# Performance work log

Measured on AMD Instinct MI355X. Metric: run time of the kernel, lower is better.

## Reference

```python
import jax, jax.numpy as jnp
import numpy as np

N, F_IN, H = 8192, 256, 64


def setup_inputs() -> dict:
    key = jax.random.key(0)
    ks = jax.random.split(key, 5)
    seq1 = jax.random.normal(ks[0], (1, N, F_IN), jnp.float32)
    seq2 = jax.random.normal(ks[1], (1, N, F_IN), jnp.float32)
    # dense (row-stochastic-ish) adjacency, batch dim 1 as in DGI usage
    adj = jax.random.uniform(ks[2], (1, N, N), jnp.float32) / np.float32(N)
    msk = jnp.ones((1, N), jnp.float32)
    # GCN params: Linear(in_ft, out_ft, bias=False) weight [H, F_IN], bias [H], PReLU alpha
    fc_w = jax.random.normal(ks[3], (H, F_IN), jnp.float32) / np.float32(np.sqrt(F_IN))
    gcn_bias = jnp.zeros((H,), jnp.float32)
    prelu_alpha = jnp.array(0.25, jnp.float32)
    # Discriminator: Bilinear(H, H, 1) -> weight [H, H], bias scalar
    disc_w = jax.random.normal(ks[4], (H, H), jnp.float32) / np.float32(np.sqrt(H))
    disc_b = jnp.zeros((1,), jnp.float32)
    return {"seq1": seq1, "seq2": seq2, "adj": adj, "msk": msk,
            "fc_w": fc_w, "gcn_bias": gcn_bias, "prelu_alpha": prelu_alpha,
            "disc_w": disc_w, "disc_b": disc_b}


def _gcn(seq, adj, fc_w, bias, alpha):
    fts = jnp.einsum('bnf,hf->bnh', seq, fc_w)          # linear, no bias
    out = jnp.einsum('bnm,bmh->bnh', adj, fts) + bias   # dense aggregation + bias
    return jnp.where(out > 0, out, alpha * out)          # PReLU


def reference(seq1, seq2, adj, msk, fc_w, gcn_bias, prelu_alpha, disc_w, disc_b):
    h1 = _gcn(seq1, adj, fc_w, gcn_bias, prelu_alpha)    # [1, N, H]
    # AvgReadout with mask: sum(seq*msk,1)/sum(msk)
    c = jnp.sum(h1 * msk[..., None], axis=1) / jnp.sum(msk)  # [1, H]
    c = jax.nn.sigmoid(c)
    h2 = _gcn(seq2, adj, fc_w, gcn_bias, prelu_alpha)    # [1, N, H]
    # Bilinear discriminator: sc[b,n] = h[b,n,:] @ W @ c[b,:] + b
    wc = jnp.einsum('hk,bk->bh', disc_w, c)              # [1, H]
    sc1 = jnp.einsum('bnh,bh->bn', h1, wc) + disc_b[0]   # [1, N]
    sc2 = jnp.einsum('bnh,bh->bn', h2, wc) + disc_b[0]   # [1, N]
    return jnp.concatenate([sc1, sc2], axis=1)           # [1, 2N]
```

## Files before the change

kernel.cpp:

```cpp
#include <hip/hip_runtime.h>
#include <cstdint>
#include <cstddef>

#define NN 8192
#define FIN 256
#define HH 64
#define SPLIT 16
#define KLEN (NN / SPLIT)

typedef float vf4 __attribute__((ext_vector_type(4)));
typedef short vbf8 __attribute__((ext_vector_type(8)));

__device__ inline unsigned pk_trunc(float lo, float hi) {
  return __builtin_amdgcn_perm(__float_as_uint(hi), __float_as_uint(lo), 0x07060302u);
}
__device__ inline unsigned short bf_rne(float x) {
  unsigned u = __float_as_uint(x);
  return (unsigned short)((u + 0x7FFFu + ((u >> 16) & 1u)) >> 16);
}
__device__ inline float bf_to_f(unsigned short s) {
  return __uint_as_float(((unsigned)s) << 16);
}

union FragU { unsigned u[4]; unsigned short s[8]; vbf8 v; };

__device__ inline vbf8 frag_trunc(vf4 a, vf4 b) {
  FragU t;
  t.u[0] = pk_trunc(a[0], a[1]);
  t.u[1] = pk_trunc(a[2], a[3]);
  t.u[2] = pk_trunc(b[0], b[1]);
  t.u[3] = pk_trunc(b[2], b[3]);
  return t.v;
}
__device__ inline vbf8 frag_rne(vf4 a, vf4 b) {
  FragU t;
  t.s[0] = bf_rne(a[0]); t.s[1] = bf_rne(a[1]); t.s[2] = bf_rne(a[2]); t.s[3] = bf_rne(a[3]);
  t.s[4] = bf_rne(b[0]); t.s[5] = bf_rne(b[1]); t.s[6] = bf_rne(b[2]); t.s[7] = bf_rne(b[3]);
  return t.v;
}

__device__ inline void gl_lds16(const void* g, void* l) {
  __builtin_amdgcn_global_load_lds(
      (const __attribute__((address_space(1))) void*)g,
      (__attribute__((address_space(3))) void*)l, 16, 0, 0);
}

__global__ __launch_bounds__(256) void k1_fts(
    const float* __restrict__ seq1, const float* __restrict__ seq2,
    const float* __restrict__ fcw, unsigned short* __restrict__ Bt,
    float* __restrict__ csum) {
  const int bx = blockIdx.x;
  const int s = bx & 1, mb = bx >> 1;
  const int wave = threadIdx.x >> 6, lane = threadIdx.x & 63;
  const int r = lane & 15, q = lane >> 4;
  const int m0 = mb * 64 + wave * 16;
  if (bx == 0 && threadIdx.x < 64) csum[threadIdx.x] = 0.f;
  const float* seq = s ? seq2 : seq1;
  const float* ap = seq + (size_t)(m0 + r) * FIN + q * 8;
  const float* bp = fcw + (size_t)r * FIN + q * 8;
  vf4 acc[4] = {};
#pragma unroll
  for (int kk = 0; kk < FIN; kk += 32) {
    vf4 a0 = *(const vf4*)ap;
    vf4 a1 = *(const vf4*)(ap + 4);
    vbf8 af = frag_rne(a0, a1);
#pragma unroll
    for (int f = 0; f < 4; ++f) {
      vf4 b0 = *(const vf4*)(bp + (size_t)f * 16 * FIN);
      vf4 b1 = *(const vf4*)(bp + (size_t)f * 16 * FIN + 4);
      vbf8 bfr = frag_rne(b0, b1);
      acc[f] = __builtin_amdgcn_mfma_f32_16x16x32_bf16(af, bfr, acc[f], 0, 0, 0);
    }
    ap += 32; bp += 32;
  }
#pragma unroll
  for (int f = 0; f < 4; ++f) {
    short4 v;
    v.x = (short)bf_rne(acc[f][0]);
    v.y = (short)bf_rne(acc[f][1]);
    v.z = (short)bf_rne(acc[f][2]);
    v.w = (short)bf_rne(acc[f][3]);
    unsigned short* dst = Bt + (size_t)(64 * s + 16 * f + r) * NN + m0 + q * 4;
    *(short4*)dst = v;
  }
}

__global__ __launch_bounds__(512, 4) void k2_agg(
    const float* __restrict__ adj, const unsigned short* __restrict__ Bt,
    unsigned short* __restrict__ Cpart) {
  constexpr int CHUNKS = KLEN / 64;
  __shared__ unsigned short lds[2][8192];
  const int bx = blockIdx.x;
  const int slice = bx & (SPLIT - 1), mb = bx / SPLIT;
  const int wave = threadIdx.x >> 6, lane = threadIdx.x & 63;
  const int r = lane & 15, q = lane >> 4;
  const int m0 = mb * 256 + wave * 32;
  const int k0 = slice * KLEN;

  auto stage = [&](int ch, int b) {
#pragma unroll
    for (int j = 0; j < 2; ++j) {
      const int g = j * 512 + wave * 64 + lane;
      const int r_ = g & 15, q_ = (g >> 4) & 3, f_ = (g >> 6) & 7, kk_ = g >> 9;
      const unsigned short* src =
          Bt + (size_t)(f_ * 16 + r_) * NN + k0 + ch * 64 + kk_ * 32 + q_ * 8;
      gl_lds16(src, &lds[b][(size_t)(j * 512 + wave * 64) * 8]);
    }
  };

  vf4 acc0[8] = {}, acc1[8] = {};
  const float* a_base0 = adj + (size_t)(m0 + r) * NN + k0 + q * 8;
  const float* a_base1 = a_base0 + (size_t)16 * NN;

  stage(0, 0);
#pragma unroll 1
  for (int ch = 0; ch < CHUNKS; ++ch) {
    __syncthreads();
    if (ch + 1 < CHUNKS) stage(ch + 1, (ch + 1) & 1);
    const int b = ch & 1;
#pragma unroll
    for (int kk = 0; kk < 2; ++kk) {
      const int kc = ch * 64 + kk * 32;
      vf4 a00 = __builtin_nontemporal_load((const vf4*)(a_base0 + kc));
      vf4 a01 = __builtin_nontemporal_load((const vf4*)(a_base0 + kc) + 1);
      vf4 a10 = __builtin_nontemporal_load((const vf4*)(a_base1 + kc));
      vf4 a11 = __builtin_nontemporal_load((const vf4*)(a_base1 + kc) + 1);
      vbf8 af0 = frag_trunc(a00, a01);
      vbf8 af1 = frag_trunc(a10, a11);
#pragma unroll
      for (int f = 0; f < 8; ++f) {
        vbf8 bfr = *(const vbf8*)&lds[b][(size_t)(kk * 512 + f * 64 + lane) * 8];
        acc0[f] = __builtin_amdgcn_mfma_f32_16x16x32_bf16(af0, bfr, acc0[f], 0, 0, 0);
        acc1[f] = __builtin_amdgcn_mfma_f32_16x16x32_bf16(af1, bfr, acc1[f], 0, 0, 0);
      }
    }
  }

#pragma unroll
  for (int f = 0; f < 8; ++f) {
    short4 v0, v1;
    v0.x = (short)bf_rne(acc0[f][0]); v0.y = (short)bf_rne(acc0[f][1]);
    v0.z = (short)bf_rne(acc0[f][2]); v0.w = (short)bf_rne(acc0[f][3]);
    v1.x = (short)bf_rne(acc1[f][0]); v1.y = (short)bf_rne(acc1[f][1]);
    v1.z = (short)bf_rne(acc1[f][2]); v1.w = (short)bf_rne(acc1[f][3]);
    unsigned short* d0 = Cpart + ((size_t)slice * 128 + f * 16 + r) * NN + m0 + q * 4;
    *(short4*)d0 = v0;
    *(short4*)(d0 + 16) = v1;
  }
}

__global__ __launch_bounds__(256) void k3_csum(
    const unsigned short* __restrict__ Cpart, const float* __restrict__ bias,
    const float* __restrict__ alpha_p, const float* __restrict__ msk,
    float* __restrict__ csum) {
  const int h = blockIdx.x >> 3, chunk = blockIdx.x & 7;
  const int t = threadIdx.x;
  const float alpha = alpha_p[0], b = bias[h];
  float sum = 0.f;
#pragma unroll
  for (int i = 0; i < 4; ++i) {
    const int m = chunk * 1024 + i * 256 + t;
    float v = 0.f;
#pragma unroll
    for (int s = 0; s < SPLIT; ++s)
      v += bf_to_f(Cpart[((size_t)s * 128 + h) * NN + m]);
    v += b;
    v = v > 0.f ? v : alpha * v;
    sum += v * msk[m];
  }
  __shared__ float red[256];
  red[t] = sum;
  __syncthreads();
  for (int off = 128; off > 32; off >>= 1) {
    if (t < off) red[t] += red[t + off];
    __syncthreads();
  }
  if (t < 32) {
    float v = red[t] + red[t + 32];
#pragma unroll
    for (int off = 16; off > 0; off >>= 1) v += __shfl_down(v, off, 64);
    if (t == 0) atomicAdd(&csum[h], v);
  }
}

__global__ __launch_bounds__(256) void k3b(
    const float* __restrict__ msk, const float* __restrict__ csum,
    const float* __restrict__ discw, float* __restrict__ wc) {
  const int t = threadIdx.x;
  __shared__ float red[256];
  __shared__ float c_sh[64];
  float ms = 0.f;
  for (int i = 0; i < 32; ++i) ms += msk[t + 256 * i];
  red[t] = ms;
  __syncthreads();
  for (int off = 128; off > 0; off >>= 1) {
    if (t < off) red[t] += red[t + off];
    __syncthreads();
  }
  if (t < 64) c_sh[t] = 1.f / (1.f + __expf(-csum[t] / red[0]));
  __syncthreads();
  if (t < 64) {
    float w = 0.f;
#pragma unroll
    for (int k = 0; k < 64; ++k) w += discw[t * 64 + k] * c_sh[k];
    wc[t] = w;
  }
}

__global__ __launch_bounds__(512) void k4_sc(
    const unsigned short* __restrict__ Cpart, const float* __restrict__ bias,
    const float* __restrict__ alpha_p, const float* __restrict__ wc,
    const float* __restrict__ discb, float* __restrict__ out) {
  const int t = threadIdx.x;
  const int ml = t & 63, g = t >> 6;
  const int m = blockIdx.x * 64 + ml;
  const float alpha = alpha_p[0];
  float sum = 0.f;
#pragma unroll
  for (int j = 0; j < 16; ++j) {
    const int n = g * 16 + j, h = n & 63;
    float v = 0.f;
#pragma unroll
    for (int s = 0; s < SPLIT; ++s)
      v += bf_to_f(Cpart[((size_t)s * 128 + n) * NN + m]);
    v += bias[h];
    v = v > 0.f ? v : alpha * v;
    sum += v * wc[h];
  }
  __shared__ float red[8][64];
  red[g][ml] = sum;
  __syncthreads();
  if (t < 128) {
    const int mm = t & 63, half = t >> 6;
    float r = red[half * 4 + 0][mm] + red[half * 4 + 1][mm] +
              red[half * 4 + 2][mm] + red[half * 4 + 3][mm];
    out[(size_t)half * NN + blockIdx.x * 64 + mm] = r + discb[0];
  }
}

extern "C" void kernel_launch(void* const* d_in, const int* in_sizes, int n_in,
                              void* d_out, int out_size, void* d_ws, size_t ws_size,
                              hipStream_t stream) {
  const float* seq1  = (const float*)d_in[0];
  const float* seq2  = (const float*)d_in[1];
  const float* adj   = (const float*)d_in[2];
  const float* msk   = (const float*)d_in[3];
  const float* fcw   = (const float*)d_in[4];
  const float* bias  = (const float*)d_in[5];
  const float* alpha = (const float*)d_in[6];
  const float* discw = (const float*)d_in[7];
  const float* discb = (const float*)d_in[8];
  float* out = (float*)d_out;
  char* ws = (char*)d_ws;

  unsigned short* Bt    = (unsigned short*)ws;
  unsigned short* Cpart = (unsigned short*)(ws + (size_t)(2 << 20));
  float* csum           = (float*)(ws + (size_t)(34 << 20));
  float* wc             = csum + 64;

  hipLaunchKernelGGL(k1_fts, dim3(256), dim3(256), 0, stream, seq1, seq2, fcw, Bt, csum);
  hipLaunchKernelGGL(k2_agg, dim3(32 * SPLIT), dim3(512), 0, stream, adj, Bt, Cpart);
  hipLaunchKernelGGL(k3_csum, dim3(512), dim3(256), 0, stream, Cpart, bias, alpha, msk, csum);
  hipLaunchKernelGGL(k3b, dim3(1), dim3(256), 0, stream, msk, csum, discw, wc);
  hipLaunchKernelGGL(k4_sc, dim3(128), dim3(512), 0, stream, Cpart, bias, alpha, wc, discb, out);
}
```

Measured before the change: 420.9 us.

## Materialize activated H once and double aggregation K-chunk per stage

The split-K partial sums are now reduced, biased and PReLU-activated once per element in k3a, which writes a compact bf16 H buffer. k4 then reads only H instead of re-reducing all 16 Cpart splits, which cuts redundant reads of the large partial buffer. Separately, k2_agg stages 128 K-columns per pipeline step instead of 64, halving barrier and loop overhead. The cost is double the LDS per block (64 KB), which may lower occupancy, plus an extra bf16 rounding of H before the discriminator dot product.

Result: faster. 412.5 us (-2.0%).

```diff
diff --git a/kernel.cpp b/kernel.cpp
--- a/kernel.cpp
+++ b/kernel.cpp
@@ -88,8 +88,8 @@
 __global__ __launch_bounds__(512, 4) void k2_agg(
     const float* __restrict__ adj, const unsigned short* __restrict__ Bt,
     unsigned short* __restrict__ Cpart) {
-  constexpr int CHUNKS = KLEN / 64;
-  __shared__ unsigned short lds[2][8192];
+  constexpr int CHUNKS = KLEN / 128;
+  __shared__ unsigned short lds[2][16384];
   const int bx = blockIdx.x;
   const int slice = bx & (SPLIT - 1), mb = bx / SPLIT;
   const int wave = threadIdx.x >> 6, lane = threadIdx.x & 63;
@@ -99,11 +99,11 @@
 
   auto stage = [&](int ch, int b) {
 #pragma unroll
-    for (int j = 0; j < 2; ++j) {
+    for (int j = 0; j < 4; ++j) {
       const int g = j * 512 + wave * 64 + lane;
       const int r_ = g & 15, q_ = (g >> 4) & 3, f_ = (g >> 6) & 7, kk_ = g >> 9;
       const unsigned short* src =
-          Bt + (size_t)(f_ * 16 + r_) * NN + k0 + ch * 64 + kk_ * 32 + q_ * 8;
+          Bt + (size_t)(f_ * 16 + r_) * NN + k0 + ch * 128 + kk_ * 32 + q_ * 8;
       gl_lds16(src, &lds[b][(size_t)(j * 512 + wave * 64) * 8]);
     }
   };
@@ -119,8 +119,8 @@
     if (ch + 1 < CHUNKS) stage(ch + 1, (ch + 1) & 1);
     const int b = ch & 1;
 #pragma unroll
-    for (int kk = 0; kk < 2; ++kk) {
-      const int kc = ch * 64 + kk * 32;
+    for (int kk = 0; kk < 4; ++kk) {
+      const int kc = ch * 128 + kk * 32;
       vf4 a00 = __builtin_nontemporal_load((const vf4*)(a_base0 + kc));
       vf4 a01 = __builtin_nontemporal_load((const vf4*)(a_base0 + kc) + 1);
       vf4 a10 = __builtin_nontemporal_load((const vf4*)(a_base1 + kc));
@@ -149,37 +149,45 @@
   }
 }
 
-__global__ __launch_bounds__(256) void k3_csum(
+__global__ __launch_bounds__(256) void k3a(
     const unsigned short* __restrict__ Cpart, const float* __restrict__ bias,
     const float* __restrict__ alpha_p, const float* __restrict__ msk,
-    float* __restrict__ csum) {
-  const int h = blockIdx.x >> 3, chunk = blockIdx.x & 7;
+    unsigned short* __restrict__ H, float* __restrict__ csum) {
+  const int n = blockIdx.x >> 2, chunk = blockIdx.x & 3;
   const int t = threadIdx.x;
-  const float alpha = alpha_p[0], b = bias[h];
-  float sum = 0.f;
-#pragma unroll
-  for (int i = 0; i < 4; ++i) {
-    const int m = chunk * 1024 + i * 256 + t;
-    float v = 0.f;
-#pragma unroll
-    for (int s = 0; s < SPLIT; ++s)
-      v += bf_to_f(Cpart[((size_t)s * 128 + h) * NN + m]);
-    v += b;
-    v = v > 0.f ? v : alpha * v;
-    sum += v * msk[m];
-  }
-  __shared__ float red[256];
-  red[t] = sum;
-  __syncthreads();
-  for (int off = 128; off > 32; off >>= 1) {
-    if (t < off) red[t] += red[t + off];
+  const int m0 = chunk * 2048 + t * 8;
+  const float alpha = alpha_p[0], b = bias[n & 63];
+  float v[8] = {};
+#pragma unroll
+  for (int s = 0; s < SPLIT; ++s) {
+    vbf8 c = *(const vbf8*)(Cpart + ((size_t)s * 128 + n) * NN + m0);
+#pragma unroll
+    for (int j = 0; j < 8; ++j) v[j] += bf_to_f((unsigned short)c[j]);
+  }
+  FragU hout;
+  float acc = 0.f;
+#pragma unroll
+  for (int j = 0; j < 8; ++j) {
+    float x = v[j] + b;
+    x = x > 0.f ? x : alpha * x;
+    hout.s[j] = bf_rne(x);
+    acc += x * msk[m0 + j];
+  }
+  *(vbf8*)(H + (size_t)n * NN + m0) = hout.v;
+  if (n < 64) {
+    __shared__ float red[256];
+    red[t] = acc;
     __syncthreads();
-  }
-  if (t < 32) {
-    float v = red[t] + red[t + 32];
-#pragma unroll
-    for (int off = 16; off > 0; off >>= 1) v += __shfl_down(v, off, 64);
-    if (t == 0) atomicAdd(&csum[h], v);
+    for (int off = 128; off > 32; off >>= 1) {
+      if (t < off) red[t] += red[t + off];
+      __syncthreads();
+    }
+    if (t < 32) {
+      float x = red[t] + red[t + 32];
+#pragma unroll
+      for (int off = 16; off > 0; off >>= 1) x += __shfl_down(x, off, 64);
+      if (t == 0) atomicAdd(&csum[n], x);
+    }
   }
 }
 
@@ -207,34 +215,24 @@
   }
 }
 
-__global__ __launch_bounds__(512) void k4_sc(
-    const unsigned short* __restrict__ Cpart, const float* __restrict__ bias,
-    const float* __restrict__ alpha_p, const float* __restrict__ wc,
+__global__ __launch_bounds__(256) void k4_sc(
+    const unsigned short* __restrict__ H, const float* __restrict__ wc,
     const float* __restrict__ discb, float* __restrict__ out) {
-  const int t = threadIdx.x;
-  const int ml = t & 63, g = t >> 6;
-  const int m = blockIdx.x * 64 + ml;
-  const float alpha = alpha_p[0];
-  float sum = 0.f;
-#pragma unroll
-  for (int j = 0; j < 16; ++j) {
-    const int n = g * 16 + j, h = n & 63;
-    float v = 0.f;
-#pragma unroll
-    for (int s = 0; s < SPLIT; ++s)
-      v += bf_to_f(Cpart[((size_t)s * 128 + n) * NN + m]);
-    v += bias[h];
-    v = v > 0.f ? v : alpha * v;
-    sum += v * wc[h];
-  }
-  __shared__ float red[8][64];
-  red[g][ml] = sum;
+  const int t = threadIdx.x, lane = t & 63, w = t >> 6;
+  const int m = blockIdx.x * 64 + lane;
+  float s = 0.f;
+#pragma unroll
+  for (int i = 0; i < 32; ++i) {
+    const int n = w * 32 + i;
+    s += bf_to_f(H[(size_t)n * NN + m]) * wc[n & 63];
+  }
+  __shared__ float red[4][64];
+  red[w][lane] = s;
   __syncthreads();
   if (t < 128) {
-    const int mm = t & 63, half = t >> 6;
-    float r = red[half * 4 + 0][mm] + red[half * 4 + 1][mm] +
-              red[half * 4 + 2][mm] + red[half * 4 + 3][mm];
-    out[(size_t)half * NN + blockIdx.x * 64 + mm] = r + discb[0];
+    const int half = t >> 6, mm = t & 63;
+    out[(size_t)half * NN + blockIdx.x * 64 + mm] =
+        red[half * 2][mm] + red[half * 2 + 1][mm] + discb[0];
   }
 }
 
@@ -255,12 +253,13 @@
 
   unsigned short* Bt    = (unsigned short*)ws;
   unsigned short* Cpart = (unsigned short*)(ws + (size_t)(2 << 20));
-  float* csum           = (float*)(ws + (size_t)(34 << 20));
+  unsigned short* H     = (unsigned short*)(ws + (size_t)(34 << 20));
+  float* csum           = (float*)(ws + (size_t)(36 << 20));
   float* wc             = csum + 64;
 
   hipLaunchKernelGGL(k1_fts, dim3(256), dim3(256), 0, stream, seq1, seq2, fcw, Bt, csum);
   hipLaunchKernelGGL(k2_agg, dim3(32 * SPLIT), dim3(512), 0, stream, adj, Bt, Cpart);
-  hipLaunchKernelGGL(k3_csum, dim3(512), dim3(256), 0, stream, Cpart, bias, alpha, msk, csum);
+  hipLaunchKernelGGL(k3a, dim3(512), dim3(256), 0, stream, Cpart, bias, alpha, msk, H, csum);
   hipLaunchKernelGGL(k3b, dim3(1), dim3(256), 0, stream, msk, csum, discw, wc);
-  hipLaunchKernelGGL(k4_sc, dim3(128), dim3(512), 0, stream, Cpart, bias, alpha, wc, discb, out);
-}
+  hipLaunchKernelGGL(k4_sc, dim3(128), dim3(256), 0, stream, H, wc, discb, out);
+}
```
